# Kernel tuning notes

Measured on AMD Instinct MI355X. Metric: run time of the kernel, lower is better.

## Reference

```python
import jax, jax.numpy as jnp
import numpy as np

D = 64          # embed_dim == latent dim
T = 200         # diffusion_steps, timestep_respacing='' -> full 200 reverse steps
B, L = 8192, 100
N_ITEMS = 100000


def setup_inputs() -> dict:
    key = jax.random.key(0)
    ks = jax.random.split(key, 16)

    def lin(k, i, o):
        return (jax.random.normal(k, (i, o), jnp.float32) / np.sqrt(i)).astype(jnp.float32)

    item_seq = jax.random.randint(ks[0], (B, L), 0, N_ITEMS)
    item_emb = jax.random.normal(ks[1], (N_ITEMS, D), jnp.float32) * 0.02
    item_emb = item_emb.at[0].set(0.0)  # padding_idx=0
    return {
        'item_seq': item_seq,
        'item_emb': item_emb,
        'W_enc1': lin(ks[2], D, 256), 'b_enc1': jnp.zeros((256,), jnp.float32),
        'W_enc2': lin(ks[3], 256, 2 * D), 'b_enc2': jnp.zeros((2 * D,), jnp.float32),
        'W_in': lin(ks[4], D, D), 'b_in': jnp.zeros((D,), jnp.float32),
        'W_t': lin(ks[5], D, D), 'b_t': jnp.zeros((D,), jnp.float32),
        'W_c': lin(ks[6], D, D), 'b_c': jnp.zeros((D,), jnp.float32),
        'W_out': lin(ks[7], D, D), 'b_out': jnp.zeros((D,), jnp.float32),
    }


def _schedule():
    # improved-diffusion linear schedule
    scale = 1000.0 / T
    betas = jnp.linspace(scale * 1e-4, scale * 0.02, T, dtype=jnp.float32)
    alphas = 1.0 - betas
    acp = jnp.cumprod(alphas)
    acp_prev = jnp.concatenate([jnp.ones((1,), jnp.float32), acp[:-1]])
    sqrt_recip = jnp.sqrt(1.0 / acp)
    sqrt_recipm1 = jnp.sqrt(1.0 / acp - 1.0)
    post_var = betas * (1.0 - acp_prev) / (1.0 - acp)
    post_logvar = jnp.log(jnp.concatenate([post_var[1:2], post_var[1:]]))  # clipped
    coef1 = betas * jnp.sqrt(acp_prev) / (1.0 - acp)
    coef2 = (1.0 - acp_prev) * jnp.sqrt(alphas) / (1.0 - acp)
    return sqrt_recip, sqrt_recipm1, post_logvar, coef1, coef2


def reference(item_seq, item_emb, W_enc1, b_enc1, W_enc2, b_enc2,
              W_in, b_in, W_t, b_t, W_c, b_c, W_out, b_out):
    # ---- pooled VAE encoder (eval mode: dropout = identity, z = mu) ----
    seq = item_emb[item_seq]                                   # [B, L, D] gather
    cnt = jnp.sum(item_seq != 0, axis=1, keepdims=True).astype(seq.dtype)
    pooled = jnp.sum(seq, axis=1) / jnp.sqrt(cnt)              # [B, D]
    h = jax.nn.relu(pooled @ W_enc1 + b_enc1)
    enc = h @ W_enc2 + b_enc2                                  # [B, 2D]
    mu, logvar = jnp.split(enc, 2, axis=-1)
    z = mu                                                     # eval reparameterize

    # ---- ScoreNet: eps-prediction MLP conditioned on x_start and sinusoidal t ----
    half = D // 2
    freqs = jnp.exp(-jnp.log(10000.0) * jnp.arange(half, dtype=jnp.float32) / half)

    def scorenet(x, t_float, cond):
        ang = t_float * freqs                                  # [D/2]
        temb = jnp.concatenate([jnp.cos(ang), jnp.sin(ang)])   # [D]
        hh = jax.nn.silu(x @ W_in + b_in + (temb @ W_t + b_t) + cond @ W_c + b_c)
        return hh @ W_out + b_out                              # eps, [B, D]

    # ---- p_sample_loop (FIXED_SMALL variance, clip_denoised=True) ----
    sqrt_recip, sqrt_recipm1, post_logvar, coef1, coef2 = _schedule()
    x_init = jax.random.normal(jax.random.key(1), z.shape, z.dtype)
    noise_key = jax.random.key(2)

    def step(x, t):
        eps = scorenet(x, t.astype(jnp.float32), z)
        x0 = jnp.clip(sqrt_recip[t] * x - sqrt_recipm1[t] * eps, -1.0, 1.0)
        mean = coef1[t] * x0 + coef2[t] * x
        noise = jax.random.normal(jax.random.fold_in(noise_key, t), x.shape, x.dtype)
        sigma = jnp.where(t > 0, jnp.exp(0.5 * post_logvar[t]), 0.0)
        return mean + sigma * noise, None

    sample, _ = jax.lax.scan(step, x_init, jnp.arange(T - 1, -1, -1))
    return sample
```

## Files before the change

### kernel.cpp

```cpp
#include <hip/hip_runtime.h>
#include <cstdint>


#define DEVI __device__ __forceinline__

typedef __attribute__((ext_vector_type(8))) short short8;
typedef __attribute__((ext_vector_type(4))) float f32x4;

DEVI uint32_t rotl32(uint32_t x, uint32_t r) { return (x << r) | (x >> (32u - r)); }

DEVI void threefry2x32(uint32_t k0, uint32_t k1, uint32_t x0, uint32_t x1,
                       uint32_t &o0, uint32_t &o1)
{
  const uint32_t ks2 = k0 ^ k1 ^ 0x1BD11BDAu;
  x0 += k0; x1 += k1;
#define TFR(r) { x0 += x1; x1 = rotl32(x1, r); x1 ^= x0; }
  TFR(13u) TFR(15u) TFR(26u) TFR(6u)   x0 += k1;  x1 += ks2 + 1u;
  TFR(17u) TFR(29u) TFR(16u) TFR(24u)  x0 += ks2; x1 += k0 + 2u;
  TFR(13u) TFR(15u) TFR(26u) TFR(6u)   x0 += k0;  x1 += k1 + 3u;
  TFR(17u) TFR(29u) TFR(16u) TFR(24u)  x0 += k1;  x1 += ks2 + 4u;
  TFR(13u) TFR(15u) TFR(26u) TFR(6u)   x0 += ks2; x1 += k0 + 5u;
#undef TFR
  o0 = x0; o1 = x1;
}

DEVI uint32_t jax_random_bits32(uint32_t k0, uint32_t k1, uint32_t j)
{
  uint32_t a, b;
  threefry2x32(k0, k1, 0u, j, a, b);
  return a ^ b;
}

DEVI float jax_bits_to_normal(uint32_t bits)
{
  const float LO = -0.99999994f;
  float f = __uint_as_float((bits >> 9) | 0x3f800000u) - 1.0f;
  float u = fmaxf(LO, f * 2.0f + LO);
  float w = -__logf((1.0f - u) * (1.0f + u));
  float p;
  if (w < 5.0f) {
    w = w - 2.5f;
    p =              2.81022636e-08f;
    p = fmaf(p, w,   3.43273939e-07f);
    p = fmaf(p, w,  -3.5233877e-06f);
    p = fmaf(p, w,  -4.39150654e-06f);
    p = fmaf(p, w,   0.00021858087f);
    p = fmaf(p, w,  -0.00125372503f);
    p = fmaf(p, w,  -0.00417768164f);
    p = fmaf(p, w,   0.246640727f);
    p = fmaf(p, w,   1.50140941f);
  } else {
    w = sqrtf(w) - 3.0f;
    p =             -0.000200214257f;
    p = fmaf(p, w,   0.000100950558f);
    p = fmaf(p, w,   0.00134934322f);
    p = fmaf(p, w,  -0.00367342844f);
    p = fmaf(p, w,   0.00573950773f);
    p = fmaf(p, w,  -0.0076224613f);
    p = fmaf(p, w,   0.00943887047f);
    p = fmaf(p, w,   1.00167406f);
    p = fmaf(p, w,   2.83297682f);
  }
  return 1.41421356237f * (p * u);
}

DEVI short bf16_hi_trunc(float x) { return (short)(__float_as_uint(x) >> 16); }
DEVI float bf16_to_f32(short h)
{
  return __uint_as_float(((uint32_t)(unsigned short)h) << 16);
}
DEVI void split_bf16(float x, short &h, short &l)
{
  h = bf16_hi_trunc(x);
  float r = x - bf16_to_f32(h);
  l = bf16_hi_trunc(r);
}

DEVI short8 ld_frag(const short* p)
{
  union { int4 v; short8 s; } u;
  const int2* q = (const int2*)p;
  int2 a = q[0], b = q[1];
  u.v = make_int4(a.x, a.y, b.x, b.y);
  return u.s;
}

__global__ __launch_bounds__(256)
void k_pool(const int* __restrict__ seq, const float* __restrict__ emb,
            float* __restrict__ pooled)
{
  const int lane = threadIdx.x & 63;
  const int r    = blockIdx.x * 4 + (threadIdx.x >> 6);
  const int* row = seq + r * 100;
  float s = 0.f;
  int cnt = 0;
  for (int l = 0; l < 100; ++l) {
    int id = row[l];
    cnt += (id != 0);
    s += emb[id * 64 + lane];
  }
  pooled[r * 64 + lane] = s / sqrtf((float)cnt);
}

__global__ __launch_bounds__(256)
void k_enc(const float* __restrict__ pooled,
           const float* __restrict__ W1, const float* __restrict__ b1,
           const float* __restrict__ W2, const float* __restrict__ b2,
           const float* __restrict__ Wc, const float* __restrict__ bc,
           float* __restrict__ cproj)
{
  __shared__ float p_s[8][64];
  __shared__ float h_s[8][256];
  __shared__ float mu_s[8][64];
  const int tid = threadIdx.x;
  const int r0  = blockIdx.x * 8;

  for (int i = tid; i < 8 * 64; i += 256)
    p_s[i >> 6][i & 63] = pooled[r0 * 64 + i];
  __syncthreads();

  float hacc[8];
#pragma unroll
  for (int r = 0; r < 8; ++r) hacc[r] = b1[tid];
  for (int k = 0; k < 64; ++k) {
    float w = W1[k * 256 + tid];
#pragma unroll
    for (int r = 0; r < 8; ++r) hacc[r] = fmaf(p_s[r][k], w, hacc[r]);
  }
#pragma unroll
  for (int r = 0; r < 8; ++r) h_s[r][tid] = fmaxf(hacc[r], 0.f);
  __syncthreads();

#pragma unroll
  for (int pass = 0; pass < 2; ++pass) {
    int r = pass * 4 + (tid >> 6);
    int j = tid & 63;
    float acc = b2[j];
    for (int k = 0; k < 256; ++k)
      acc = fmaf(h_s[r][k], W2[k * 128 + j], acc);
    mu_s[r][j] = acc;
  }
  __syncthreads();

#pragma unroll
  for (int pass = 0; pass < 2; ++pass) {
    int r = pass * 4 + (tid >> 6);
    int j = tid & 63;
    float acc = bc[j];
    for (int k = 0; k < 64; ++k)
      acc = fmaf(mu_s[r][k], Wc[k * 64 + j], acc);
    cproj[(r0 + r) * 64 + j] = acc;
  }
}

__global__ __launch_bounds__(64)
void k_prep(const float* __restrict__ Wt, const float* __restrict__ bt,
            const float* __restrict__ bin, float* __restrict__ tpb,
            float* __restrict__ sched)
{
  __shared__ float temb[64];
  const int t = blockIdx.x;
  const int d = threadIdx.x;
  const float lg = logf(10000.0f);
  {
    int i = d & 31;
    float fr  = expf((-lg * (float)i) / 32.0f);
    float ang = (float)t * fr;
    temb[d] = (d < 32) ? cosf(ang) : sinf(ang);
  }
  if (d == 0) {
    const float start = (float)(5.0 * 1e-4);
    const float stop  = (float)(5.0 * 0.02);
    const float delta = stop - start;
    float prod = 1.f, acp_prev = 1.f, beta = 0.f, alpha = 1.f;
    for (int i = 0; i <= t; ++i) {
      beta  = start + ((float)i * delta) / 199.0f;
      alpha = 1.0f - beta;
      acp_prev = prod;
      prod = prod * alpha;
    }
    float acp = prod;
    float om  = 1.0f - acp;
    sched[t * 8 + 0] = sqrtf(1.0f / acp);
    sched[t * 8 + 1] = sqrtf(1.0f / acp - 1.0f);
    sched[t * 8 + 2] = beta * sqrtf(acp_prev) / om;
    sched[t * 8 + 3] = (1.0f - acp_prev) * sqrtf(alpha) / om;
    float pv = beta * (1.0f - acp_prev) / om;
    sched[t * 8 + 4] = (t > 0) ? sqrtf(pv) : 0.0f;
    uint32_t fk0, fk1;
    threefry2x32(0u, 2u, 0u, (uint32_t)t, fk0, fk1);
    ((uint32_t*)sched)[t * 8 + 5] = fk0;
    ((uint32_t*)sched)[t * 8 + 6] = fk1;
  }
  __syncthreads();
  float acc = bt[d] + bin[d];
  for (int k = 0; k < 64; ++k)
    acc = fmaf(temb[k], Wt[k * 64 + d], acc);
  tpb[t * 64 + d] = acc;
}

#define WLDW  68
#define XLDW  68
#define PACCW 10

__global__ __launch_bounds__(512, 4)
void k_ddpm(const float* __restrict__ Win, const float* __restrict__ Wout,
            const float* __restrict__ bout,
            const float* __restrict__ cproj, const float* __restrict__ tpb,
            const float* __restrict__ sched, float* __restrict__ out)
{
  __shared__ short WiHs[64 * WLDW], WiLs[64 * WLDW];
  __shared__ short WoHs[64 * WLDW], WoLs[64 * WLDW];
  __shared__ short Xh[16 * XLDW], Xl[16 * XLDW], Hh[16 * XLDW], Hl[16 * XLDW];
  __shared__ float pacc[2 * 64 * PACCW];

  const int tid  = threadIdx.x;
  const int lane = tid & 63;
  const int w    = tid >> 6;
  const int nt   = w & 3;
  const int kc   = w >> 2;
  const int nn   = lane & 15;
  const int quad = lane >> 4;
  const int dim  = nt * 16 + nn;
  const int arow = nn;
  const int r0g  = blockIdx.x * 16;
  const int kofs = kc * 32 + quad * 8;
  const int rA   = quad * 4 + 2 * kc;

  for (int idx = tid; idx < 4096; idx += 512) {
    int k = idx >> 6, n = idx & 63;
    short h, l;
    split_bf16(Win[idx], h, l);
    WiHs[n * WLDW + k] = h; WiLs[n * WLDW + k] = l;
    split_bf16(Wout[idx], h, l);
    WoHs[n * WLDW + k] = h; WoLs[n * WLDW + k] = l;
  }

  const float bo = bout[dim];
  const uint32_t jA = (uint32_t)((r0g + rA) * 64 + dim);
  const uint32_t jB = jA + 64u;
  const float cpA = cproj[jA];
  const float cpB = cproj[jB];

  float xoA = jax_bits_to_normal(jax_random_bits32(0u, 1u, jA));
  float xoB = jax_bits_to_normal(jax_random_bits32(0u, 1u, jB));
  {
    short h, l;
    split_bf16(xoA, h, l); Xh[rA * XLDW + dim] = h; Xl[rA * XLDW + dim] = l;
    split_bf16(xoB, h, l); Xh[(rA+1) * XLDW + dim] = h; Xl[(rA+1) * XLDW + dim] = l;
  }
  __syncthreads();

  float tp = tpb[199 * 64 + dim];

  float* pacc_w = &pacc[(kc * 64 + dim) * PACCW + quad * 2];
  const float* pacc_r = &pacc[((1 - kc) * 64 + dim) * PACCW + quad * 2];

#pragma unroll 1
  for (int t = 199; t >= 0; --t) {
    const float sr   = sched[t * 8 + 0];
    const float srm1 = sched[t * 8 + 1];
    const float c1   = sched[t * 8 + 2];
    const float c2   = sched[t * 8 + 3];
    const float sg   = sched[t * 8 + 4];
    const uint32_t fk0 = ((const uint32_t*)sched)[t * 8 + 5];
    const uint32_t fk1 = ((const uint32_t*)sched)[t * 8 + 6];

    float nA = jax_bits_to_normal(jax_random_bits32(fk0, fk1, jA));
    float nB = jax_bits_to_normal(jax_random_bits32(fk0, fk1, jB));

    f32x4 acc;
    if (kc == 0) { acc[0] = tp + cpA; acc[1] = tp + cpB; acc[2] = 0.f; acc[3] = 0.f; }
    else         { acc[0] = 0.f; acc[1] = 0.f; acc[2] = tp + cpA; acc[3] = tp + cpB; }
    {
      short8 ah = ld_frag(&Xh[arow * XLDW + kofs]);
      short8 al = ld_frag(&Xl[arow * XLDW + kofs]);
      short8 bh = ld_frag(&WiHs[dim * WLDW + kofs]);
      short8 bl = ld_frag(&WiLs[dim * WLDW + kofs]);
      acc = __builtin_amdgcn_mfma_f32_16x16x32_bf16(al, bh, acc, 0, 0, 0);
      acc = __builtin_amdgcn_mfma_f32_16x16x32_bf16(ah, bl, acc, 0, 0, 0);
      acc = __builtin_amdgcn_mfma_f32_16x16x32_bf16(ah, bh, acc, 0, 0, 0);
    }
    if (kc == 0) *(float2*)pacc_w = make_float2(acc[2], acc[3]);
    else         *(float2*)pacc_w = make_float2(acc[0], acc[1]);
    __syncthreads();

    {
      float2 o = *(const float2*)pacc_r;
      float vA, vB;
      if (kc == 0) { vA = acc[0] + o.x; vB = acc[1] + o.y; }
      else         { vA = acc[2] + o.x; vB = acc[3] + o.y; }
      vA = vA * __builtin_amdgcn_rcpf(1.0f + __expf(-vA));
      vB = vB * __builtin_amdgcn_rcpf(1.0f + __expf(-vB));
      short h, l;
      split_bf16(vA, h, l); Hh[rA * XLDW + dim] = h; Hl[rA * XLDW + dim] = l;
      split_bf16(vB, h, l); Hh[(rA+1) * XLDW + dim] = h; Hl[(rA+1) * XLDW + dim] = l;
    }
    int tn = (t > 0) ? (t - 1) : 0;
    float tpn = tpb[tn * 64 + dim];
    __syncthreads();

    f32x4 eac;
    if (kc == 0) { eac[0] = bo; eac[1] = bo; eac[2] = 0.f; eac[3] = 0.f; }
    else         { eac[0] = 0.f; eac[1] = 0.f; eac[2] = bo; eac[3] = bo; }
    {
      short8 ah = ld_frag(&Hh[arow * XLDW + kofs]);
      short8 al = ld_frag(&Hl[arow * XLDW + kofs]);
      short8 bh = ld_frag(&WoHs[dim * WLDW + kofs]);
      short8 bl = ld_frag(&WoLs[dim * WLDW + kofs]);
      eac = __builtin_amdgcn_mfma_f32_16x16x32_bf16(al, bh, eac, 0, 0, 0);
      eac = __builtin_amdgcn_mfma_f32_16x16x32_bf16(ah, bl, eac, 0, 0, 0);
      eac = __builtin_amdgcn_mfma_f32_16x16x32_bf16(ah, bh, eac, 0, 0, 0);
    }
    if (kc == 0) *(float2*)pacc_w = make_float2(eac[2], eac[3]);
    else         *(float2*)pacc_w = make_float2(eac[0], eac[1]);
    __syncthreads();

    {
      float2 o = *(const float2*)pacc_r;
      float eA, eB;
      if (kc == 0) { eA = eac[0] + o.x; eB = eac[1] + o.y; }
      else         { eA = eac[2] + o.x; eB = eac[3] + o.y; }
      float xcA = fminf(1.f, fmaxf(-1.f, sr * xoA - srm1 * eA));
      float xcB = fminf(1.f, fmaxf(-1.f, sr * xoB - srm1 * eB));
      xoA = c1 * xcA + c2 * xoA + sg * nA;
      xoB = c1 * xcB + c2 * xoB + sg * nB;
      short h, l;
      split_bf16(xoA, h, l); Xh[rA * XLDW + dim] = h; Xl[rA * XLDW + dim] = l;
      split_bf16(xoB, h, l); Xh[(rA+1) * XLDW + dim] = h; Xl[(rA+1) * XLDW + dim] = l;
      tp = tpn;
    }
    __syncthreads();
  }

  out[jA] = xoA;
  out[jB] = xoB;
}

extern "C" void kernel_launch(void* const* d_in, const int* in_sizes, int n_in,
                              void* d_out, int out_size, void* d_ws, size_t ws_size,
                              hipStream_t stream)
{
  const int*   seq  = (const int*)  d_in[0];
  const float* emb  = (const float*)d_in[1];
  const float* W1   = (const float*)d_in[2];
  const float* b1   = (const float*)d_in[3];
  const float* W2   = (const float*)d_in[4];
  const float* b2   = (const float*)d_in[5];
  const float* Win  = (const float*)d_in[6];
  const float* bin  = (const float*)d_in[7];
  const float* Wt   = (const float*)d_in[8];
  const float* bt   = (const float*)d_in[9];
  const float* Wc   = (const float*)d_in[10];
  const float* bc   = (const float*)d_in[11];
  const float* Wout = (const float*)d_in[12];
  const float* bout = (const float*)d_in[13];

  float* out   = (float*)d_out;
  float* ws    = (float*)d_ws;
  float* cproj = ws;
  float* tpb   = ws + 524288;
  float* sched = ws + 524288 + 12800;
  float* pooled = out;

  k_pool <<<2048, 256, 0, stream>>>(seq, emb, pooled);
  k_enc  <<<1024, 256, 0, stream>>>(pooled, W1, b1, W2, b2, Wc, bc, cproj);
  k_prep <<<200, 64, 0, stream>>>(Wt, bt, bin, tpb, sched);
  k_ddpm <<<512, 512, 0, stream>>>(Win, Wout, bout, cproj, tpb, sched, out);
}
```

Measured before the change: 608.6 us.

## Warp-specialize DDPM loop: producer waves generate next-step noise while compute waves run MFMA

```diff
diff --git a/kernel.cpp b/kernel.cpp
--- a/kernel.cpp
+++ b/kernel.cpp
@@ -7,14 +7,12 @@
 typedef __attribute__((ext_vector_type(8))) short short8;
 typedef __attribute__((ext_vector_type(4))) float f32x4;
 
-DEVI uint32_t rotl32(uint32_t x, uint32_t r) { return (x << r) | (x >> (32u - r)); }
-
 DEVI void threefry2x32(uint32_t k0, uint32_t k1, uint32_t x0, uint32_t x1,
                        uint32_t &o0, uint32_t &o1)
 {
   const uint32_t ks2 = k0 ^ k1 ^ 0x1BD11BDAu;
   x0 += k0; x1 += k1;
-#define TFR(r) { x0 += x1; x1 = rotl32(x1, r); x1 ^= x0; }
+#define TFR(r) { x0 += x1; x1 = __builtin_rotateleft32(x1, r); x1 ^= x0; }
   TFR(13u) TFR(15u) TFR(26u) TFR(6u)   x0 += k1;  x1 += ks2 + 1u;
   TFR(17u) TFR(29u) TFR(16u) TFR(24u)  x0 += ks2; x1 += k0 + 2u;
   TFR(13u) TFR(15u) TFR(26u) TFR(6u)   x0 += k0;  x1 += k1 + 3u;
@@ -203,7 +201,8 @@
 #define XLDW  68
 #define PACCW 10
 
-__global__ __launch_bounds__(512, 4)
+__global__
+__attribute__((amdgpu_flat_work_group_size(1024, 1024), amdgpu_waves_per_eu(8)))
 void k_ddpm(const float* __restrict__ Win, const float* __restrict__ Wout,
             const float* __restrict__ bout,
             const float* __restrict__ cproj, const float* __restrict__ tpb,
@@ -213,21 +212,16 @@
   __shared__ short WoHs[64 * WLDW], WoLs[64 * WLDW];
   __shared__ short Xh[16 * XLDW], Xl[16 * XLDW], Hh[16 * XLDW], Hl[16 * XLDW];
   __shared__ float pacc[2 * 64 * PACCW];
+  __shared__ float nbuf[2 * 1024];
 
   const int tid  = threadIdx.x;
   const int lane = tid & 63;
   const int w    = tid >> 6;
-  const int nt   = w & 3;
-  const int kc   = w >> 2;
-  const int nn   = lane & 15;
-  const int quad = lane >> 4;
-  const int dim  = nt * 16 + nn;
-  const int arow = nn;
+  const bool isCompute = (w & 1) == 0;
   const int r0g  = blockIdx.x * 16;
-  const int kofs = kc * 32 + quad * 8;
-  const int rA   = quad * 4 + 2 * kc;
-
-  for (int idx = tid; idx < 4096; idx += 512) {
+  const uint32_t* su = (const uint32_t*)sched;
+
+  for (int idx = tid; idx < 4096; idx += 1024) {
     int k = idx >> 6, n = idx & 63;
     short h, l;
     split_bf16(Win[idx], h, l);
@@ -236,56 +230,89 @@
     WoHs[n * WLDW + k] = h; WoLs[n * WLDW + k] = l;
   }
 
-  const float bo = bout[dim];
-  const uint32_t jA = (uint32_t)((r0g + rA) * 64 + dim);
-  const uint32_t jB = jA + 64u;
-  const float cpA = cproj[jA];
-  const float cpB = cproj[jB];
-
-  float xoA = jax_bits_to_normal(jax_random_bits32(0u, 1u, jA));
-  float xoB = jax_bits_to_normal(jax_random_bits32(0u, 1u, jB));
-  {
+  const int cw   = w >> 1;
+  const int nt   = cw & 3;
+  const int kc   = cw >> 2;
+  const int nn   = lane & 15;
+  const int quad = lane >> 4;
+  const int dim  = nt * 16 + nn;
+  const int arow = nn;
+  const int kofs = kc * 32 + quad * 8;
+  const int rA   = quad * 4 + 2 * kc;
+
+  const int nw = w >> 1;
+  const uint32_t jn0 = (uint32_t)((r0g + 2 * nw) * 64 + lane);
+  const uint32_t jn1 = jn0 + 64u;
+  const int wi0 = 2 * nw * 64 + lane;
+  const int wi1 = wi0 + 64;
+
+  float xoA = 0.f, xoB = 0.f, cpA = 0.f, cpB = 0.f, bo = 0.f, tp = 0.f;
+  uint32_t jA = 0, jB = 0;
+  float* pacc_w = nullptr;
+  const float* pacc_r = nullptr;
+
+  if (isCompute) {
+    bo  = bout[dim];
+    jA  = (uint32_t)((r0g + rA) * 64 + dim);
+    jB  = jA + 64u;
+    cpA = cproj[jA];
+    cpB = cproj[jB];
+    xoA = jax_bits_to_normal(jax_random_bits32(0u, 1u, jA));
+    xoB = jax_bits_to_normal(jax_random_bits32(0u, 1u, jB));
     short h, l;
     split_bf16(xoA, h, l); Xh[rA * XLDW + dim] = h; Xl[rA * XLDW + dim] = l;
     split_bf16(xoB, h, l); Xh[(rA+1) * XLDW + dim] = h; Xl[(rA+1) * XLDW + dim] = l;
+    tp = tpb[199 * 64 + dim];
+    pacc_w = &pacc[(kc * 64 + dim) * PACCW + quad * 2];
+    pacc_r = &pacc[((1 - kc) * 64 + dim) * PACCW + quad * 2];
+  } else {
+    uint32_t gk0 = su[199 * 8 + 5];
+    uint32_t gk1 = su[199 * 8 + 6];
+    nbuf[1024 + wi0] = jax_bits_to_normal(jax_random_bits32(gk0, gk1, jn0));
+    nbuf[1024 + wi1] = jax_bits_to_normal(jax_random_bits32(gk0, gk1, jn1));
   }
   __syncthreads();
-
-  float tp = tpb[199 * 64 + dim];
-
-  float* pacc_w = &pacc[(kc * 64 + dim) * PACCW + quad * 2];
-  const float* pacc_r = &pacc[((1 - kc) * 64 + dim) * PACCW + quad * 2];
 
 #pragma unroll 1
   for (int t = 199; t >= 0; --t) {
-    const float sr   = sched[t * 8 + 0];
-    const float srm1 = sched[t * 8 + 1];
-    const float c1   = sched[t * 8 + 2];
-    const float c2   = sched[t * 8 + 3];
-    const float sg   = sched[t * 8 + 4];
-    const uint32_t fk0 = ((const uint32_t*)sched)[t * 8 + 5];
-    const uint32_t fk1 = ((const uint32_t*)sched)[t * 8 + 6];
-
-    float nA = jax_bits_to_normal(jax_random_bits32(fk0, fk1, jA));
-    float nB = jax_bits_to_normal(jax_random_bits32(fk0, fk1, jB));
-
+    float nA = 0.f, nB = 0.f;
+    float sr = 0.f, srm1 = 0.f, c1 = 0.f, c2 = 0.f, sg = 0.f;
     f32x4 acc;
-    if (kc == 0) { acc[0] = tp + cpA; acc[1] = tp + cpB; acc[2] = 0.f; acc[3] = 0.f; }
-    else         { acc[0] = 0.f; acc[1] = 0.f; acc[2] = tp + cpA; acc[3] = tp + cpB; }
-    {
-      short8 ah = ld_frag(&Xh[arow * XLDW + kofs]);
-      short8 al = ld_frag(&Xl[arow * XLDW + kofs]);
-      short8 bh = ld_frag(&WiHs[dim * WLDW + kofs]);
-      short8 bl = ld_frag(&WiLs[dim * WLDW + kofs]);
-      acc = __builtin_amdgcn_mfma_f32_16x16x32_bf16(al, bh, acc, 0, 0, 0);
-      acc = __builtin_amdgcn_mfma_f32_16x16x32_bf16(ah, bl, acc, 0, 0, 0);
-      acc = __builtin_amdgcn_mfma_f32_16x16x32_bf16(ah, bh, acc, 0, 0, 0);
+    uint32_t gk0 = 0, gk1 = 0;
+    float* ndst = nullptr;
+
+    if (isCompute) {
+      sr   = sched[t * 8 + 0];
+      srm1 = sched[t * 8 + 1];
+      c1   = sched[t * 8 + 2];
+      c2   = sched[t * 8 + 3];
+      sg   = sched[t * 8 + 4];
+      const float* nb = nbuf + (t & 1) * 1024;
+      nA = nb[rA * 64 + dim];
+      nB = nb[rA * 64 + 64 + dim];
+
+      if (kc == 0) { acc[0] = tp + cpA; acc[1] = tp + cpB; acc[2] = 0.f; acc[3] = 0.f; }
+      else         { acc[0] = 0.f; acc[1] = 0.f; acc[2] = tp + cpA; acc[3] = tp + cpB; }
+      {
+        short8 ah = ld_frag(&Xh[arow * XLDW + kofs]);
+        short8 al = ld_frag(&Xl[arow * XLDW + kofs]);
+        short8 bh = ld_frag(&WiHs[dim * WLDW + kofs]);
+        short8 bl = ld_frag(&WiLs[dim * WLDW + kofs]);
+        acc = __builtin_amdgcn_mfma_f32_16x16x32_bf16(al, bh, acc, 0, 0, 0);
+        acc = __builtin_amdgcn_mfma_f32_16x16x32_bf16(ah, bl, acc, 0, 0, 0);
+        acc = __builtin_amdgcn_mfma_f32_16x16x32_bf16(ah, bh, acc, 0, 0, 0);
+      }
+      if (kc == 0) *(float2*)pacc_w = make_float2(acc[2], acc[3]);
+      else         *(float2*)pacc_w = make_float2(acc[0], acc[1]);
+    } else if (t > 0) {
+      gk0 = su[(t - 1) * 8 + 5];
+      gk1 = su[(t - 1) * 8 + 6];
+      ndst = nbuf + ((t - 1) & 1) * 1024;
+      ndst[wi0] = jax_bits_to_normal(jax_random_bits32(gk0, gk1, jn0));
     }
-    if (kc == 0) *(float2*)pacc_w = make_float2(acc[2], acc[3]);
-    else         *(float2*)pacc_w = make_float2(acc[0], acc[1]);
     __syncthreads();
 
-    {
+    if (isCompute) {
       float2 o = *(const float2*)pacc_r;
       float vA, vB;
       if (kc == 0) { vA = acc[0] + o.x; vB = acc[1] + o.y; }
@@ -295,28 +322,32 @@
       short h, l;
       split_bf16(vA, h, l); Hh[rA * XLDW + dim] = h; Hl[rA * XLDW + dim] = l;
       split_bf16(vB, h, l); Hh[(rA+1) * XLDW + dim] = h; Hl[(rA+1) * XLDW + dim] = l;
+    } else if (t > 0) {
+      ndst[wi1] = jax_bits_to_normal(jax_random_bits32(gk0, gk1, jn1));
     }
     int tn = (t > 0) ? (t - 1) : 0;
-    float tpn = tpb[tn * 64 + dim];
+    float tpn = isCompute ? tpb[tn * 64 + dim] : 0.f;
     __syncthreads();
 
     f32x4 eac;
-    if (kc == 0) { eac[0] = bo; eac[1] = bo; eac[2] = 0.f; eac[3] = 0.f; }
-    else         { eac[0] = 0.f; eac[1] = 0.f; eac[2] = bo; eac[3] = bo; }
-    {
-      short8 ah = ld_frag(&Hh[arow * XLDW + kofs]);
-      short8 al = ld_frag(&Hl[arow * XLDW + kofs]);
-      short8 bh = ld_frag(&WoHs[dim * WLDW + kofs]);
-      short8 bl = ld_frag(&WoLs[dim * WLDW + kofs]);
-      eac = __builtin_amdgcn_mfma_f32_16x16x32_bf16(al, bh, eac, 0, 0, 0);
-      eac = __builtin_amdgcn_mfma_f32_16x16x32_bf16(ah, bl, eac, 0, 0, 0);
-      eac = __builtin_amdgcn_mfma_f32_16x16x32_bf16(ah, bh, eac, 0, 0, 0);
+    if (isCompute) {
+      if (kc == 0) { eac[0] = bo; eac[1] = bo; eac[2] = 0.f; eac[3] = 0.f; }
+      else         { eac[0] = 0.f; eac[1] = 0.f; eac[2] = bo; eac[3] = bo; }
+      {
+        short8 ah = ld_frag(&Hh[arow * XLDW + kofs]);
+        short8 al = ld_frag(&Hl[arow * XLDW + kofs]);
+        short8 bh = ld_frag(&WoHs[dim * WLDW + kofs]);
+        short8 bl = ld_frag(&WoLs[dim * WLDW + kofs]);
+        eac = __builtin_amdgcn_mfma_f32_16x16x32_bf16(al, bh, eac, 0, 0, 0);
+        eac = __builtin_amdgcn_mfma_f32_16x16x32_bf16(ah, bl, eac, 0, 0, 0);
+        eac = __builtin_amdgcn_mfma_f32_16x16x32_bf16(ah, bh, eac, 0, 0, 0);
+      }
+      if (kc == 0) *(float2*)pacc_w = make_float2(eac[2], eac[3]);
+      else         *(float2*)pacc_w = make_float2(eac[0], eac[1]);
     }
-    if (kc == 0) *(float2*)pacc_w = make_float2(eac[2], eac[3]);
-    else         *(float2*)pacc_w = make_float2(eac[0], eac[1]);
     __syncthreads();
 
-    {
+    if (isCompute) {
       float2 o = *(const float2*)pacc_r;
       float eA, eB;
       if (kc == 0) { eA = eac[0] + o.x; eB = eac[1] + o.y; }
@@ -333,8 +364,10 @@
     __syncthreads();
   }
 
-  out[jA] = xoA;
-  out[jB] = xoB;
+  if (isCompute) {
+    out[jA] = xoA;
+    out[jB] = xoB;
+  }
 }
 
 extern "C" void kernel_launch(void* const* d_in, const int* in_sizes, int n_in,
@@ -366,5 +399,5 @@
   k_pool <<<2048, 256, 0, stream>>>(seq, emb, pooled);
   k_enc  <<<1024, 256, 0, stream>>>(pooled, W1, b1, W2, b2, Wc, bc, cproj);
   k_prep <<<200, 64, 0, stream>>>(Wt, bt, bin, tpb, sched);
-  k_ddpm <<<512, 512, 0, stream>>>(Win, Wout, bout, cproj, tpb, sched, out);
-}
+  k_ddpm <<<512, 1024, 0, stream>>>(Win, Wout, bout, cproj, tpb, sched, out);
+}
```

After: 784.7 us. 28.9% more time.

## Drop split-K reduction in DDPM loop so each wave computes full K

Applied to the files above, without the earlier changes.

```diff
diff --git a/kernel.cpp b/kernel.cpp
--- a/kernel.cpp
+++ b/kernel.cpp
@@ -7,14 +7,12 @@
 typedef __attribute__((ext_vector_type(8))) short short8;
 typedef __attribute__((ext_vector_type(4))) float f32x4;
 
-DEVI uint32_t rotl32(uint32_t x, uint32_t r) { return (x << r) | (x >> (32u - r)); }
-
 DEVI void threefry2x32(uint32_t k0, uint32_t k1, uint32_t x0, uint32_t x1,
                        uint32_t &o0, uint32_t &o1)
 {
   const uint32_t ks2 = k0 ^ k1 ^ 0x1BD11BDAu;
   x0 += k0; x1 += k1;
-#define TFR(r) { x0 += x1; x1 = rotl32(x1, r); x1 ^= x0; }
+#define TFR(r) { x0 += x1; x1 = __builtin_rotateleft32(x1, r); x1 ^= x0; }
   TFR(13u) TFR(15u) TFR(26u) TFR(6u)   x0 += k1;  x1 += ks2 + 1u;
   TFR(17u) TFR(29u) TFR(16u) TFR(24u)  x0 += ks2; x1 += k0 + 2u;
   TFR(13u) TFR(15u) TFR(26u) TFR(6u)   x0 += k0;  x1 += k1 + 3u;
@@ -76,12 +74,10 @@
   l = bf16_hi_trunc(r);
 }
 
-DEVI short8 ld_frag(const short* p)
+DEVI short8 ld_frag16(const short* p)
 {
   union { int4 v; short8 s; } u;
-  const int2* q = (const int2*)p;
-  int2 a = q[0], b = q[1];
-  u.v = make_int4(a.x, a.y, b.x, b.y);
+  u.v = *(const int4*)p;
   return u.s;
 }
 
@@ -199,20 +195,20 @@
   tpb[t * 64 + d] = acc;
 }
 
-#define WLDW  68
-#define XLDW  68
-#define PACCW 10
-
-__global__ __launch_bounds__(512, 4)
+#define WLDW  72
+#define XLDW  72
+
+__global__
+__attribute__((amdgpu_flat_work_group_size(512, 512), amdgpu_waves_per_eu(4, 4)))
 void k_ddpm(const float* __restrict__ Win, const float* __restrict__ Wout,
             const float* __restrict__ bout,
             const float* __restrict__ cproj, const float* __restrict__ tpb,
             const float* __restrict__ sched, float* __restrict__ out)
 {
-  __shared__ short WiHs[64 * WLDW], WiLs[64 * WLDW];
-  __shared__ short WoHs[64 * WLDW], WoLs[64 * WLDW];
-  __shared__ short Xh[16 * XLDW], Xl[16 * XLDW], Hh[16 * XLDW], Hl[16 * XLDW];
-  __shared__ float pacc[2 * 64 * PACCW];
+  __shared__ __align__(16) short WiHs[64 * WLDW], WiLs[64 * WLDW];
+  __shared__ __align__(16) short WoHs[64 * WLDW], WoLs[64 * WLDW];
+  __shared__ __align__(16) short Xh[16 * XLDW], Xl[16 * XLDW];
+  __shared__ __align__(16) short Hh[16 * XLDW], Hl[16 * XLDW];
 
   const int tid  = threadIdx.x;
   const int lane = tid & 63;
@@ -224,7 +220,8 @@
   const int dim  = nt * 16 + nn;
   const int arow = nn;
   const int r0g  = blockIdx.x * 16;
-  const int kofs = kc * 32 + quad * 8;
+  const int kq0  = quad * 8;
+  const int kq1  = 32 + quad * 8;
   const int rA   = quad * 4 + 2 * kc;
 
   for (int idx = tid; idx < 4096; idx += 512) {
@@ -252,9 +249,6 @@
   __syncthreads();
 
   float tp = tpb[199 * 64 + dim];
-
-  float* pacc_w = &pacc[(kc * 64 + dim) * PACCW + quad * 2];
-  const float* pacc_r = &pacc[((1 - kc) * 64 + dim) * PACCW + quad * 2];
 
 #pragma unroll 1
   for (int t = 199; t >= 0; --t) {
@@ -273,23 +267,25 @@
     if (kc == 0) { acc[0] = tp + cpA; acc[1] = tp + cpB; acc[2] = 0.f; acc[3] = 0.f; }
     else         { acc[0] = 0.f; acc[1] = 0.f; acc[2] = tp + cpA; acc[3] = tp + cpB; }
     {
-      short8 ah = ld_frag(&Xh[arow * XLDW + kofs]);
-      short8 al = ld_frag(&Xl[arow * XLDW + kofs]);
-      short8 bh = ld_frag(&WiHs[dim * WLDW + kofs]);
-      short8 bl = ld_frag(&WiLs[dim * WLDW + kofs]);
-      acc = __builtin_amdgcn_mfma_f32_16x16x32_bf16(al, bh, acc, 0, 0, 0);
-      acc = __builtin_amdgcn_mfma_f32_16x16x32_bf16(ah, bl, acc, 0, 0, 0);
-      acc = __builtin_amdgcn_mfma_f32_16x16x32_bf16(ah, bh, acc, 0, 0, 0);
-    }
-    if (kc == 0) *(float2*)pacc_w = make_float2(acc[2], acc[3]);
-    else         *(float2*)pacc_w = make_float2(acc[0], acc[1]);
-    __syncthreads();
-
+      short8 xh0 = ld_frag16(&Xh[arow * XLDW + kq0]);
+      short8 xl0 = ld_frag16(&Xl[arow * XLDW + kq0]);
+      short8 wh0 = ld_frag16(&WiHs[dim * WLDW + kq0]);
+      short8 wl0 = ld_frag16(&WiLs[dim * WLDW + kq0]);
+      short8 xh1 = ld_frag16(&Xh[arow * XLDW + kq1]);
+      short8 xl1 = ld_frag16(&Xl[arow * XLDW + kq1]);
+      short8 wh1 = ld_frag16(&WiHs[dim * WLDW + kq1]);
+      short8 wl1 = ld_frag16(&WiLs[dim * WLDW + kq1]);
+      acc = __builtin_amdgcn_mfma_f32_16x16x32_bf16(xl0, wh0, acc, 0, 0, 0);
+      acc = __builtin_amdgcn_mfma_f32_16x16x32_bf16(xh0, wl0, acc, 0, 0, 0);
+      acc = __builtin_amdgcn_mfma_f32_16x16x32_bf16(xh0, wh0, acc, 0, 0, 0);
+      acc = __builtin_amdgcn_mfma_f32_16x16x32_bf16(xl1, wh1, acc, 0, 0, 0);
+      acc = __builtin_amdgcn_mfma_f32_16x16x32_bf16(xh1, wl1, acc, 0, 0, 0);
+      acc = __builtin_amdgcn_mfma_f32_16x16x32_bf16(xh1, wh1, acc, 0, 0, 0);
+    }
     {
-      float2 o = *(const float2*)pacc_r;
       float vA, vB;
-      if (kc == 0) { vA = acc[0] + o.x; vB = acc[1] + o.y; }
-      else         { vA = acc[2] + o.x; vB = acc[3] + o.y; }
+      if (kc == 0) { vA = acc[0]; vB = acc[1]; }
+      else         { vA = acc[2]; vB = acc[3]; }
       vA = vA * __builtin_amdgcn_rcpf(1.0f + __expf(-vA));
       vB = vB * __builtin_amdgcn_rcpf(1.0f + __expf(-vB));
       short h, l;
@@ -304,23 +300,25 @@
     if (kc == 0) { eac[0] = bo; eac[1] = bo; eac[2] = 0.f; eac[3] = 0.f; }
     else         { eac[0] = 0.f; eac[1] = 0.f; eac[2] = bo; eac[3] = bo; }
     {
-      short8 ah = ld_frag(&Hh[arow * XLDW + kofs]);
-      short8 al = ld_frag(&Hl[arow * XLDW + kofs]);
-      short8 bh = ld_frag(&WoHs[dim * WLDW + kofs]);
-      short8 bl = ld_frag(&WoLs[dim * WLDW + kofs]);
-      eac = __builtin_amdgcn_mfma_f32_16x16x32_bf16(al, bh, eac, 0, 0, 0);
-      eac = __builtin_amdgcn_mfma_f32_16x16x32_bf16(ah, bl, eac, 0, 0, 0);
-      eac = __builtin_amdgcn_mfma_f32_16x16x32_bf16(ah, bh, eac, 0, 0, 0);
-    }
-    if (kc == 0) *(float2*)pacc_w = make_float2(eac[2], eac[3]);
-    else         *(float2*)pacc_w = make_float2(eac[0], eac[1]);
-    __syncthreads();
-
+      short8 hh0 = ld_frag16(&Hh[arow * XLDW + kq0]);
+      short8 hl0 = ld_frag16(&Hl[arow * XLDW + kq0]);
+      short8 wh0 = ld_frag16(&WoHs[dim * WLDW + kq0]);
+      short8 wl0 = ld_frag16(&WoLs[dim * WLDW + kq0]);
+      short8 hh1 = ld_frag16(&Hh[arow * XLDW + kq1]);
+      short8 hl1 = ld_frag16(&Hl[arow * XLDW + kq1]);
+      short8 wh1 = ld_frag16(&WoHs[dim * WLDW + kq1]);
+      short8 wl1 = ld_frag16(&WoLs[dim * WLDW + kq1]);
+      eac = __builtin_amdgcn_mfma_f32_16x16x32_bf16(hl0, wh0, eac, 0, 0, 0);
+      eac = __builtin_amdgcn_mfma_f32_16x16x32_bf16(hh0, wl0, eac, 0, 0, 0);
+      eac = __builtin_amdgcn_mfma_f32_16x16x32_bf16(hh0, wh0, eac, 0, 0, 0);
+      eac = __builtin_amdgcn_mfma_f32_16x16x32_bf16(hl1, wh1, eac, 0, 0, 0);
+      eac = __builtin_amdgcn_mfma_f32_16x16x32_bf16(hh1, wl1, eac, 0, 0, 0);
+      eac = __builtin_amdgcn_mfma_f32_16x16x32_bf16(hh1, wh1, eac, 0, 0, 0);
+    }
     {
-      float2 o = *(const float2*)pacc_r;
       float eA, eB;
-      if (kc == 0) { eA = eac[0] + o.x; eB = eac[1] + o.y; }
-      else         { eA = eac[2] + o.x; eB = eac[3] + o.y; }
+      if (kc == 0) { eA = eac[0]; eB = eac[1]; }
+      else         { eA = eac[2]; eB = eac[3]; }
       float xcA = fminf(1.f, fmaxf(-1.f, sr * xoA - srm1 * eA));
       float xcB = fminf(1.f, fmaxf(-1.f, sr * xoB - srm1 * eB));
       xoA = c1 * xcA + c2 * xoA + sg * nA;
```

Result: faster. 591.5 us (-2.8%).
